# Kernel optimization log

Hardware: AMD Instinct MI355X
Metric: run time of the kernel (lower is better)

The kernel has to match this reference:

```python
import jax, jax.numpy as jnp
import numpy as np
import math

B, T, C = 4, 2048, 1024
N_HEADS = 16
D_HEAD = C // N_HEADS


def _rope_tables(d_head, max_seq_len):
    half = d_head // 2
    theta = 1.0 / (10000.0 ** (jnp.arange(half, dtype=jnp.float32) / half))
    pos = jnp.arange(max_seq_len, dtype=jnp.float32)
    freqs = jnp.outer(pos, theta)  # [S, half]
    cos = jnp.concatenate([jnp.cos(freqs), jnp.cos(freqs)], axis=-1)  # [S, d_head]
    sin = jnp.concatenate([jnp.sin(freqs), jnp.sin(freqs)], axis=-1)
    return cos, sin


def _rotate_half(x):
    d = x.shape[-1] // 2
    return jnp.concatenate([-x[..., d:], x[..., :d]], axis=-1)


def _apply_rope(x, cos, sin):
    # x: [B, H, T, d_head]; cos/sin: [T, d_head] broadcast over B,H
    return x * cos[None, None] + _rotate_half(x) * sin[None, None]


def setup_inputs() -> dict:
    key = jax.random.key(0)
    k1, k2, k3 = jax.random.split(key, 3)
    x = jax.random.normal(k1, (B, T, C), dtype=jnp.float32)
    W_qkv = jax.random.normal(k2, (C, 3 * C), dtype=jnp.float32) * (1.0 / math.sqrt(C))
    W_proj = jax.random.normal(k3, (C, C), dtype=jnp.float32) * (1.0 / math.sqrt(C))
    return {"x": x, "W_qkv": W_qkv, "W_proj": W_proj}


def reference(x, W_qkv, W_proj):
    b, t, c = x.shape
    qkv = x @ W_qkv  # [B, T, 3C]
    q, k, v = jnp.split(qkv, 3, axis=-1)

    def reshape(z):
        return z.reshape(b, t, N_HEADS, D_HEAD).transpose(0, 2, 1, 3)  # [B,H,T,dh]

    q, k, v = reshape(q), reshape(k), reshape(v)

    cos, sin = _rope_tables(D_HEAD, t)
    q = _apply_rope(q, cos, sin)
    k = _apply_rope(k, cos, sin)

    scale = 1.0 / math.sqrt(D_HEAD)
    att = jnp.einsum('bhqd,bhkd->bhqk', q, k) * scale  # [B,H,T,T]
    causal = jnp.tril(jnp.ones((t, t), dtype=bool))
    att = jnp.where(causal[None, None], att, -jnp.inf)
    att = jax.nn.softmax(att, axis=-1)
    out = jnp.einsum('bhqk,bhkd->bhqd', att, v)  # [B,H,T,dh]
    out = out.transpose(0, 2, 1, 3).reshape(b, t, c)
    return out @ W_proj
```

## Files before the change

kernel.cpp:

```cpp
#include <hip/hip_runtime.h>
#include <stdint.h>

#define Bz 4
#define Tz 2048
#define Cz 1024
#define NHz 16
#define DHz 64
#define Mz (Bz*Tz)

typedef unsigned short u16;
typedef __attribute__((ext_vector_type(8))) short short8;
typedef __attribute__((ext_vector_type(8))) unsigned short ushort8v;
typedef __attribute__((ext_vector_type(4))) unsigned short u16x4;
typedef __attribute__((ext_vector_type(4))) float f32x4;
typedef __attribute__((ext_vector_type(2))) unsigned int uint2v;

__device__ __forceinline__ float bf2f(u16 u){
  union { unsigned int i; float f; } v; v.i = ((unsigned int)u) << 16; return v.f;
}
__device__ __forceinline__ u16 f2bf(float f){
  union { float f; unsigned int i; } v; v.f = f;
  unsigned int r = v.i + 0x7FFFu + ((v.i >> 16) & 1u);
  return (u16)(r >> 16);
}


__global__ void k_cast_bf16(const float* __restrict__ in, u16* __restrict__ out, int n4){
  int i = blockIdx.x*256 + threadIdx.x;
  if (i >= n4) return;
  float4 v = ((const float4*)in)[i];
  u16x4 o;
  o[0] = f2bf(v.x); o[1] = f2bf(v.y); o[2] = f2bf(v.z); o[3] = f2bf(v.w);
  *(u16x4*)(out + (size_t)i*4) = o;
}

__global__ void k_transpose_cast(const float* __restrict__ W, u16* __restrict__ Wt, int K, int N){
  __shared__ float tile[32][33];
  int n0 = blockIdx.x*32, k0 = blockIdx.y*32;
  int tx = threadIdx.x, ty = threadIdx.y;
  #pragma unroll
  for (int i = 0; i < 32; i += 8)
    tile[ty+i][tx] = W[(size_t)(k0+ty+i)*N + n0 + tx];
  __syncthreads();
  #pragma unroll
  for (int i = 0; i < 32; i += 8)
    Wt[(size_t)(n0+ty+i)*K + k0 + tx] = f2bf(tile[tx][ty+i]);
}

__global__ void k_rope_tables(float* __restrict__ cosT, float* __restrict__ sinT){
  int idx = blockIdx.x*256 + threadIdx.x;
  int t = idx >> 5, i = idx & 31;
  float theta = exp2f(-(float)i * (13.287712379549449f / 32.0f));
  float ang = (float)t * theta;
  cosT[idx] = cosf(ang);
  sinT[idx] = sinf(ang);
}

#define GLDS(src, dstE) __builtin_amdgcn_global_load_lds( \
    (const __attribute__((address_space(1))) unsigned int*)(src), \
    (__attribute__((address_space(3))) unsigned int*)((u16*)lds + (dstE)), 16, 0, 0)

template<int Nn, int Kk, bool ROPE>
__global__ __launch_bounds__(256, 4) void k_gemmdb(const u16* __restrict__ A, const u16* __restrict__ Bt,
                        void* __restrict__ Cout, u16* __restrict__ vTout,
                        const float* __restrict__ cosT, const float* __restrict__ sinT){
  __shared__ u16 lds[2][16384];
  constexpr int NT = Kk/64;
  const int bm = blockIdx.x, bn = blockIdx.y;
  const int tid = threadIdx.x, lane = tid & 63, w = tid >> 6;
  const int wm = (w >> 1)*64, wn = (w & 1)*64;
  const int g = lane >> 4, r = lane & 15;

  const int srow8 = lane >> 3;
  const int sslot = (lane & 7) ^ srow8;
  const u16* asrc = A  + (size_t)(bm*128 + w*32 + srow8)*Kk + sslot*8;
  const u16* bsrc = Bt + (size_t)(bn*128 + w*32 + srow8)*Kk + sslot*8;
  const int dA = w*2048 + lane*8;
  const int dB = 8192 + w*2048 + lane*8;

  int a_off[4][2], b_off[4][2];
  #pragma unroll
  for (int i = 0; i < 4; ++i)
    #pragma unroll
    for (int kc = 0; kc < 2; ++kc){
      int row = wm + i*16 + r;
      a_off[i][kc] = (row*128 + kc*64 + g*16) ^ ((r & 7) << 4);
      int rowb = wn + i*16 + r;
      b_off[i][kc] = 16384 + ((rowb*128 + kc*64 + g*16) ^ ((r & 7) << 4));
    }

  f32x4 acc[4][4] = {};

#define STG(t, bi) do{ \
    const size_t ko_ = (size_t)(t)*64; \
    const int be_ = (bi)*16384; \
    GLDS(asrc + ko_,                 be_ + dA);        \
    GLDS(asrc + ko_ +  8*(size_t)Kk, be_ + dA + 512);  \
    GLDS(asrc + ko_ + 16*(size_t)Kk, be_ + dA + 1024); \
    GLDS(asrc + ko_ + 24*(size_t)Kk, be_ + dA + 1536); \
    GLDS(bsrc + ko_,                 be_ + dB);        \
    GLDS(bsrc + ko_ +  8*(size_t)Kk, be_ + dB + 512);  \
    GLDS(bsrc + ko_ + 16*(size_t)Kk, be_ + dB + 1024); \
    GLDS(bsrc + ko_ + 24*(size_t)Kk, be_ + dB + 1536); \
  }while(0)

  STG(0, 0);
  asm volatile("s_waitcnt vmcnt(0)" ::: "memory");
  __builtin_amdgcn_s_barrier();

  int buf = 0;
  #pragma unroll 1
  for (int t = 0; t < NT; ++t){
    if (t + 1 < NT) STG(t+1, buf^1);
    const char* Lb = (const char*)lds + buf*32768;
    short8 af[4][2], bf[4][2];
    #pragma unroll
    for (int i = 0; i < 4; ++i)
      #pragma unroll
      for (int kc = 0; kc < 2; ++kc){
        af[i][kc] = *(const short8*)(Lb + a_off[i][kc]);
        bf[i][kc] = *(const short8*)(Lb + b_off[i][kc]);
      }
    __builtin_amdgcn_s_setprio(1);
    #pragma unroll
    for (int i = 0; i < 4; ++i)
      #pragma unroll
      for (int j = 0; j < 4; ++j){
        acc[i][j] = __builtin_amdgcn_mfma_f32_16x16x32_bf16(af[i][0], bf[j][0], acc[i][j], 0,0,0);
        acc[i][j] = __builtin_amdgcn_mfma_f32_16x16x32_bf16(af[i][1], bf[j][1], acc[i][j], 0,0,0);
      }
    __builtin_amdgcn_s_setprio(0);
    if (t + 1 < NT){
      asm volatile("s_waitcnt vmcnt(0)" ::: "memory");
      __builtin_amdgcn_s_barrier();
      buf ^= 1;
    }
  }
#undef STG

  const int nbase = bn*128 + wn;
  if (ROPE && nbase >= 2048){
    const int b = bm >> 4;
    const int h = (nbase >> 6) & 15;
    #pragma unroll
    for (int ri = 0; ri < 4; ++ri){
      const int m0 = bm*128 + wm + ri*16 + 4*g;
      const int t0 = m0 & (Tz-1);
      #pragma unroll
      for (int cj = 0; cj < 4; ++cj){
        const int d = cj*16 + r;
        u16x4 o;
        #pragma unroll
        for (int jj = 0; jj < 4; ++jj) o[jj] = f2bf(acc[ri][cj][jj]);
        *(u16x4*)(vTout + ((size_t)((b*16 + h)*64 + d))*2048 + t0) = o;
      }
    }
  } else if (ROPE){
    const float qs = (nbase < 1024) ? 0.18033688011112042f : 1.0f;
    #pragma unroll
    for (int ri = 0; ri < 4; ++ri)
      #pragma unroll
      for (int jj = 0; jj < 4; ++jj){
        const int m = bm*128 + wm + ri*16 + 4*g + jj;
        const int t = m & (Tz-1);
        #pragma unroll
        for (int cj = 0; cj < 2; ++cj){
          const int ch = cj*16 + r;
          float cv = cosT[t*32 + ch];
          float sv = sinT[t*32 + ch];
          float lo = acc[ri][cj][jj], hi = acc[ri][cj+2][jj];
          ((u16*)Cout)[(size_t)m*Nn + nbase + ch]      = f2bf((lo*cv - hi*sv)*qs);
          ((u16*)Cout)[(size_t)m*Nn + nbase + ch + 32] = f2bf((hi*cv + lo*sv)*qs);
        }
      }
  } else {
    #pragma unroll
    for (int ri = 0; ri < 4; ++ri)
      #pragma unroll
      for (int cj = 0; cj < 4; ++cj)
        #pragma unroll
        for (int jj = 0; jj < 4; ++jj){
          const size_t m = bm*128 + wm + ri*16 + 4*g + jj;
          const size_t n = (size_t)nbase + cj*16 + r;
          ((float*)Cout)[m*Nn + n] = acc[ri][cj][jj];
        }
  }
}

__global__ __launch_bounds__(512) void k_attn2(const u16* __restrict__ qkv,
                                               const u16* __restrict__ vT,
                                               u16* __restrict__ att){
  __shared__ u16 K_lds[2*4096];
  __shared__ u16 V_lds[2*4096];
  __shared__ u16 P_lds[8*16*72];

  const int bh = blockIdx.x;
  const int b = bh >> 4, h = bh & 15;
  const int tid = threadIdx.x;
  const int w = tid >> 6;
  const int lane = tid & 63;
  const int g = lane >> 4;
  const int ql = lane & 15;
  u16* Pw = P_lds + w*16*72;

  const int srow  = lane >> 3;
  const int sslot = (lane & 7) ^ srow;
  const u16* ksrc = qkv + ((size_t)(b*Tz + 8*w + srow))*3072 + 1024 + h*64 + sslot*8;
  const u16* vsrc = vT  + ((size_t)bh*64 + 8*w + srow)*2048 + sslot*8;
  u16* kdst = K_lds + w*512 + lane*8;
  u16* vdst = V_lds + w*512 + lane*8;

  short8 ones;
  #pragma unroll
  for (int i = 0; i < 8; ++i) ones[i] = (short)0x3F80;

  int fofs[4][2];
  #pragma unroll
  for (int t = 0; t < 4; ++t){
    int row = 16*t + ql;
    fofs[t][0] = (row*128 + 16*g)      ^ ((row & 7) << 4);
    fofs[t][1] = (row*128 + 64 + 16*g) ^ ((row & 7) << 4);
  }

  #pragma unroll 1
  for (int half = 0; half < 2; ++half){
    const int qt = (half == 0) ? blockIdx.y : (15 - blockIdx.y);
    const int qr0w = qt*128 + w*16;
    const int nt = 2*qt + 2;

    const u16* qsrc = qkv + (size_t)(b*Tz + qr0w + ql)*3072 + h*64;
    short8 qf0 = *(const short8*)(qsrc + g*8);
    short8 qf1 = *(const short8*)(qsrc + 32 + g*8);

    f32x4 acc[4] = {{0,0,0,0},{0,0,0,0},{0,0,0,0},{0,0,0,0}};
    f32x4 accl = {0,0,0,0};

    __builtin_amdgcn_global_load_lds(
      (const __attribute__((address_space(1))) unsigned int*)(ksrc),
      (__attribute__((address_space(3))) unsigned int*)(kdst), 16, 0, 0);
    __builtin_amdgcn_global_load_lds(
      (const __attribute__((address_space(1))) unsigned int*)(vsrc),
      (__attribute__((address_space(3))) unsigned int*)(vdst), 16, 0, 0);
    __syncthreads();

    #pragma unroll 2
    for (int kt = 0; kt < nt; ++kt){
      const int buf = kt & 1;
      if (kt + 1 < nt){
        __builtin_amdgcn_global_load_lds(
          (const __attribute__((address_space(1))) unsigned int*)(ksrc + (size_t)(kt+1)*64*3072),
          (__attribute__((address_space(3))) unsigned int*)(kdst + (buf^1)*4096), 16, 0, 0);
        __builtin_amdgcn_global_load_lds(
          (const __attribute__((address_space(1))) unsigned int*)(vsrc + (kt+1)*64),
          (__attribute__((address_space(3))) unsigned int*)(vdst + (buf^1)*4096), 16, 0, 0);
      }
      const char* Kb = (const char*)(K_lds + buf*4096);
      const char* Vb = (const char*)(V_lds + buf*4096);
      const int kv0 = kt*64;

      f32x4 st[4];
      __builtin_amdgcn_s_setprio(1);
      #pragma unroll
      for (int t = 0; t < 4; ++t){
        short8 kf0 = *(const short8*)(Kb + fofs[t][0]);
        short8 kf1 = *(const short8*)(Kb + fofs[t][1]);
        f32x4 z = {0,0,0,0};
        z = __builtin_amdgcn_mfma_f32_16x16x32_bf16(kf0, qf0, z, 0, 0, 0);
        z = __builtin_amdgcn_mfma_f32_16x16x32_bf16(kf1, qf1, z, 0, 0, 0);
        st[t] = z;
      }
      __builtin_amdgcn_s_setprio(0);

      if (kv0 + 63 > qr0w){
        const int qg = qr0w + ql;
        #pragma unroll
        for (int t = 0; t < 4; ++t)
          #pragma unroll
          for (int j = 0; j < 4; ++j)
            if (kv0 + 16*t + 4*g + j > qg) st[t][j] = -1e30f;
      }

      #pragma unroll
      for (int t = 0; t < 4; ++t){
        float p0, p1, p2, p3;
        asm("v_exp_f32 %0, %1" : "=v"(p0) : "v"(st[t][0]));
        asm("v_exp_f32 %0, %1" : "=v"(p1) : "v"(st[t][1]));
        asm("v_exp_f32 %0, %1" : "=v"(p2) : "v"(st[t][2]));
        asm("v_exp_f32 %0, %1" : "=v"(p3) : "v"(st[t][3]));
        unsigned int lov, hiv;
        asm("v_cvt_pk_bf16_f32 %0, %1, %2" : "=v"(lov) : "v"(p0), "v"(p1));
        asm("v_cvt_pk_bf16_f32 %0, %1, %2" : "=v"(hiv) : "v"(p2), "v"(p3));
        uint2v pv; pv[0] = lov; pv[1] = hiv;
        *(uint2v*)((char*)Pw + ql*144 + (16*t + 4*g)*2) = pv;
      }

      short8 pf0 = *(const short8*)((char*)Pw + ql*144 + 16*g);
      short8 pf1 = *(const short8*)((char*)Pw + ql*144 + 64 + 16*g);
      __builtin_amdgcn_s_setprio(1);
      accl = __builtin_amdgcn_mfma_f32_16x16x32_bf16(pf0, ones, accl, 0, 0, 0);
      accl = __builtin_amdgcn_mfma_f32_16x16x32_bf16(pf1, ones, accl, 0, 0, 0);
      #pragma unroll
      for (int dt = 0; dt < 4; ++dt){
        short8 vf0 = *(const short8*)(Vb + fofs[dt][0]);
        short8 vf1 = *(const short8*)(Vb + fofs[dt][1]);
        acc[dt] = __builtin_amdgcn_mfma_f32_16x16x32_bf16(pf0, vf0, acc[dt], 0, 0, 0);
        acc[dt] = __builtin_amdgcn_mfma_f32_16x16x32_bf16(pf1, vf1, acc[dt], 0, 0, 0);
      }
      __builtin_amdgcn_s_setprio(0);
      __syncthreads();
    }

    float lj[4];
    #pragma unroll
    for (int j = 0; j < 4; ++j) lj[j] = 1.0f / accl[j];
    #pragma unroll
    for (int dt = 0; dt < 4; ++dt)
      #pragma unroll
      for (int j = 0; j < 4; ++j)
        att[(size_t)(b*Tz + qr0w + 4*g + j)*Cz + h*64 + dt*16 + ql] = f2bf(acc[dt][j]*lj[j]);
  }
}


extern "C" void kernel_launch(void* const* d_in, const int* in_sizes, int n_in,
                              void* d_out, int out_size, void* d_ws, size_t ws_size,
                              hipStream_t stream){
  const float* x     = (const float*)d_in[0];
  const float* Wqkv  = (const float*)d_in[1];
  const float* Wproj = (const float*)d_in[2];
  float* out = (float*)d_out;
  char* ws = (char*)d_ws;

  u16*  xb   = (u16*)(ws);
  u16*  wqt  = (u16*)(ws + 16777216);
  u16*  wpt  = (u16*)(ws + 23068672);
  u16*  qkv  = (u16*)(ws + 25165824);
  u16*  vTr  = (u16*)(ws + 75497472);
  float* cosT = (float*)(ws + 92274688);
  float* sinT = (float*)(ws + 92536832);

  k_cast_bf16<<<Mz*Cz/4/256, 256, 0, stream>>>(x, xb, Mz*Cz/4);
  k_transpose_cast<<<dim3(3072/32, 1024/32), dim3(32,8), 0, stream>>>(Wqkv, wqt, 1024, 3072);
  k_transpose_cast<<<dim3(1024/32, 1024/32), dim3(32,8), 0, stream>>>(Wproj, wpt, 1024, 1024);
  k_rope_tables<<<Tz*32/256, 256, 0, stream>>>(cosT, sinT);

  k_gemmdb<3072, 1024, true><<<dim3(Mz/128, 3072/128), 256, 0, stream>>>(
      xb, wqt, qkv, vTr, cosT, sinT);
  k_attn2<<<dim3(Bz*NHz, 8), 512, 0, stream>>>(qkv, vTr, xb);
  k_gemmdb<1024, 1024, false><<<dim3(Mz/128, 1024/128), 256, 0, stream>>>(
      xb, wpt, out, nullptr, nullptr, nullptr);
}
```

Before: 157.9 us.

## Process two 16-row query tiles per wave and compute softmax row sums with VALU

The attention kernel now runs 256 threads (4 waves), and each wave handles 32 query rows as two 16-row MFMA tiles that share every K and V fragment read from LDS. The ones-vector MFMA that produced softmax row sums is replaced by per-lane VALU adds followed by cross-lane shuffles at the end. The aim is to halve LDS fragment traffic per unit of MFMA work and to drop the extra MFMAs. In exchange the kernel uses more registers and has fewer waves per block, which could reduce latency hiding.

```diff
diff --git a/kernel.cpp b/kernel.cpp
--- a/kernel.cpp
+++ b/kernel.cpp
@@ -187,12 +187,12 @@
   }
 }
 
-__global__ __launch_bounds__(512) void k_attn2(const u16* __restrict__ qkv,
+__global__ __launch_bounds__(256) void k_attn3(const u16* __restrict__ qkv,
                                                const u16* __restrict__ vT,
                                                u16* __restrict__ att){
   __shared__ u16 K_lds[2*4096];
   __shared__ u16 V_lds[2*4096];
-  __shared__ u16 P_lds[8*16*72];
+  __shared__ u16 P_lds[4*32*72];
 
   const int bh = blockIdx.x;
   const int b = bh >> 4, h = bh & 15;
@@ -201,18 +201,14 @@
   const int lane = tid & 63;
   const int g = lane >> 4;
   const int ql = lane & 15;
-  u16* Pw = P_lds + w*16*72;
+  u16* Pw = P_lds + w*32*72;
 
   const int srow  = lane >> 3;
   const int sslot = (lane & 7) ^ srow;
-  const u16* ksrc = qkv + ((size_t)(b*Tz + 8*w + srow))*3072 + 1024 + h*64 + sslot*8;
-  const u16* vsrc = vT  + ((size_t)bh*64 + 8*w + srow)*2048 + sslot*8;
-  u16* kdst = K_lds + w*512 + lane*8;
-  u16* vdst = V_lds + w*512 + lane*8;
-
-  short8 ones;
-  #pragma unroll
-  for (int i = 0; i < 8; ++i) ones[i] = (short)0x3F80;
+  const u16* ksrc = qkv + ((size_t)(b*Tz + 16*w + srow))*3072 + 1024 + h*64 + sslot*8;
+  const u16* vsrc = vT  + ((size_t)bh*64 + 16*w + srow)*2048 + sslot*8;
+  u16* kdst = K_lds + w*1024 + lane*8;
+  u16* vdst = V_lds + w*1024 + lane*8;
 
   int fofs[4][2];
   #pragma unroll
@@ -222,52 +218,63 @@
     fofs[t][1] = (row*128 + 64 + 16*g) ^ ((row & 7) << 4);
   }
 
+#define STG_KV(kt, bi) do{ \
+    const u16* ks_ = ksrc + (size_t)(kt)*64*3072; \
+    const u16* vs_ = vsrc + (kt)*64; \
+    u16* kd_ = kdst + (bi)*4096; \
+    u16* vd_ = vdst + (bi)*4096; \
+    __builtin_amdgcn_global_load_lds((const __attribute__((address_space(1))) unsigned int*)(ks_), \
+        (__attribute__((address_space(3))) unsigned int*)(kd_), 16, 0, 0); \
+    __builtin_amdgcn_global_load_lds((const __attribute__((address_space(1))) unsigned int*)(ks_ + 8*3072), \
+        (__attribute__((address_space(3))) unsigned int*)(kd_ + 512), 16, 0, 0); \
+    __builtin_amdgcn_global_load_lds((const __attribute__((address_space(1))) unsigned int*)(vs_), \
+        (__attribute__((address_space(3))) unsigned int*)(vd_), 16, 0, 0); \
+    __builtin_amdgcn_global_load_lds((const __attribute__((address_space(1))) unsigned int*)(vs_ + 8*2048), \
+        (__attribute__((address_space(3))) unsigned int*)(vd_ + 512), 16, 0, 0); \
+  }while(0)
+
   #pragma unroll 1
   for (int half = 0; half < 2; ++half){
     const int qt = (half == 0) ? blockIdx.y : (15 - blockIdx.y);
-    const int qr0w = qt*128 + w*16;
+    const int qr0w = qt*128 + w*32;
     const int nt = 2*qt + 2;
 
-    const u16* qsrc = qkv + (size_t)(b*Tz + qr0w + ql)*3072 + h*64;
-    short8 qf0 = *(const short8*)(qsrc + g*8);
-    short8 qf1 = *(const short8*)(qsrc + 32 + g*8);
-
-    f32x4 acc[4] = {{0,0,0,0},{0,0,0,0},{0,0,0,0},{0,0,0,0}};
-    f32x4 accl = {0,0,0,0};
-
-    __builtin_amdgcn_global_load_lds(
-      (const __attribute__((address_space(1))) unsigned int*)(ksrc),
-      (__attribute__((address_space(3))) unsigned int*)(kdst), 16, 0, 0);
-    __builtin_amdgcn_global_load_lds(
-      (const __attribute__((address_space(1))) unsigned int*)(vsrc),
-      (__attribute__((address_space(3))) unsigned int*)(vdst), 16, 0, 0);
+    const u16* qsrcA = qkv + (size_t)(b*Tz + qr0w + ql)*3072 + h*64;
+    const u16* qsrcB = qsrcA + 16*3072;
+    short8 qfA0 = *(const short8*)(qsrcA + g*8);
+    short8 qfA1 = *(const short8*)(qsrcA + 32 + g*8);
+    short8 qfB0 = *(const short8*)(qsrcB + g*8);
+    short8 qfB1 = *(const short8*)(qsrcB + 32 + g*8);
+
+    f32x4 accA[4] = {{0,0,0,0},{0,0,0,0},{0,0,0,0},{0,0,0,0}};
+    f32x4 accB[4] = {{0,0,0,0},{0,0,0,0},{0,0,0,0},{0,0,0,0}};
+    float lrA = 0.0f, lrB = 0.0f;
+
+    STG_KV(0, 0);
     __syncthreads();
 
     #pragma unroll 2
     for (int kt = 0; kt < nt; ++kt){
       const int buf = kt & 1;
-      if (kt + 1 < nt){
-        __builtin_amdgcn_global_load_lds(
-          (const __attribute__((address_space(1))) unsigned int*)(ksrc + (size_t)(kt+1)*64*3072),
-          (__attribute__((address_space(3))) unsigned int*)(kdst + (buf^1)*4096), 16, 0, 0);
-        __builtin_amdgcn_global_load_lds(
-          (const __attribute__((address_space(1))) unsigned int*)(vsrc + (kt+1)*64),
-          (__attribute__((address_space(3))) unsigned int*)(vdst + (buf^1)*4096), 16, 0, 0);
-      }
+      if (kt + 1 < nt) STG_KV(kt+1, buf^1);
       const char* Kb = (const char*)(K_lds + buf*4096);
       const char* Vb = (const char*)(V_lds + buf*4096);
       const int kv0 = kt*64;
 
-      f32x4 st[4];
+      f32x4 stA[4], stB[4];
       __builtin_amdgcn_s_setprio(1);
       #pragma unroll
       for (int t = 0; t < 4; ++t){
         short8 kf0 = *(const short8*)(Kb + fofs[t][0]);
         short8 kf1 = *(const short8*)(Kb + fofs[t][1]);
-        f32x4 z = {0,0,0,0};
-        z = __builtin_amdgcn_mfma_f32_16x16x32_bf16(kf0, qf0, z, 0, 0, 0);
-        z = __builtin_amdgcn_mfma_f32_16x16x32_bf16(kf1, qf1, z, 0, 0, 0);
-        st[t] = z;
+        f32x4 zA = {0,0,0,0};
+        zA = __builtin_amdgcn_mfma_f32_16x16x32_bf16(kf0, qfA0, zA, 0, 0, 0);
+        zA = __builtin_amdgcn_mfma_f32_16x16x32_bf16(kf1, qfA1, zA, 0, 0, 0);
+        stA[t] = zA;
+        f32x4 zB = {0,0,0,0};
+        zB = __builtin_amdgcn_mfma_f32_16x16x32_bf16(kf0, qfB0, zB, 0, 0, 0);
+        zB = __builtin_amdgcn_mfma_f32_16x16x32_bf16(kf1, qfB1, zB, 0, 0, 0);
+        stB[t] = zB;
       }
       __builtin_amdgcn_s_setprio(0);
 
@@ -277,48 +284,80 @@
         for (int t = 0; t < 4; ++t)
           #pragma unroll
           for (int j = 0; j < 4; ++j)
-            if (kv0 + 16*t + 4*g + j > qg) st[t][j] = -1e30f;
+            if (kv0 + 16*t + 4*g + j > qg) stA[t][j] = -1e30f;
+      }
+      if (kv0 + 63 > qr0w + 16){
+        const int qg = qr0w + 16 + ql;
+        #pragma unroll
+        for (int t = 0; t < 4; ++t)
+          #pragma unroll
+          for (int j = 0; j < 4; ++j)
+            if (kv0 + 16*t + 4*g + j > qg) stB[t][j] = -1e30f;
       }
 
       #pragma unroll
       for (int t = 0; t < 4; ++t){
-        float p0, p1, p2, p3;
-        asm("v_exp_f32 %0, %1" : "=v"(p0) : "v"(st[t][0]));
-        asm("v_exp_f32 %0, %1" : "=v"(p1) : "v"(st[t][1]));
-        asm("v_exp_f32 %0, %1" : "=v"(p2) : "v"(st[t][2]));
-        asm("v_exp_f32 %0, %1" : "=v"(p3) : "v"(st[t][3]));
-        unsigned int lov, hiv;
-        asm("v_cvt_pk_bf16_f32 %0, %1, %2" : "=v"(lov) : "v"(p0), "v"(p1));
-        asm("v_cvt_pk_bf16_f32 %0, %1, %2" : "=v"(hiv) : "v"(p2), "v"(p3));
-        uint2v pv; pv[0] = lov; pv[1] = hiv;
-        *(uint2v*)((char*)Pw + ql*144 + (16*t + 4*g)*2) = pv;
-      }
-
-      short8 pf0 = *(const short8*)((char*)Pw + ql*144 + 16*g);
-      short8 pf1 = *(const short8*)((char*)Pw + ql*144 + 64 + 16*g);
+        float a0, a1, a2, a3, b0, b1, b2, b3;
+        asm("v_exp_f32 %0, %1" : "=v"(a0) : "v"(stA[t][0]));
+        asm("v_exp_f32 %0, %1" : "=v"(a1) : "v"(stA[t][1]));
+        asm("v_exp_f32 %0, %1" : "=v"(a2) : "v"(stA[t][2]));
+        asm("v_exp_f32 %0, %1" : "=v"(a3) : "v"(stA[t][3]));
+        asm("v_exp_f32 %0, %1" : "=v"(b0) : "v"(stB[t][0]));
+        asm("v_exp_f32 %0, %1" : "=v"(b1) : "v"(stB[t][1]));
+        asm("v_exp_f32 %0, %1" : "=v"(b2) : "v"(stB[t][2]));
+        asm("v_exp_f32 %0, %1" : "=v"(b3) : "v"(stB[t][3]));
+        lrA += (a0+a1)+(a2+a3);
+        lrB += (b0+b1)+(b2+b3);
+        unsigned int wa0, wa1, wb0, wb1;
+        asm("v_cvt_pk_bf16_f32 %0, %1, %2" : "=v"(wa0) : "v"(a0), "v"(a1));
+        asm("v_cvt_pk_bf16_f32 %0, %1, %2" : "=v"(wa1) : "v"(a2), "v"(a3));
+        asm("v_cvt_pk_bf16_f32 %0, %1, %2" : "=v"(wb0) : "v"(b0), "v"(b1));
+        asm("v_cvt_pk_bf16_f32 %0, %1, %2" : "=v"(wb1) : "v"(b2), "v"(b3));
+        uint2v pva; pva[0] = wa0; pva[1] = wa1;
+        uint2v pvb; pvb[0] = wb0; pvb[1] = wb1;
+        *(uint2v*)((char*)Pw + ql*144 + (16*t + 4*g)*2) = pva;
+        *(uint2v*)((char*)Pw + (16 + ql)*144 + (16*t + 4*g)*2) = pvb;
+      }
+
+      short8 pfA0 = *(const short8*)((char*)Pw + ql*144 + 16*g);
+      short8 pfA1 = *(const short8*)((char*)Pw + ql*144 + 64 + 16*g);
+      short8 pfB0 = *(const short8*)((char*)Pw + (16 + ql)*144 + 16*g);
+      short8 pfB1 = *(const short8*)((char*)Pw + (16 + ql)*144 + 64 + 16*g);
+
       __builtin_amdgcn_s_setprio(1);
-      accl = __builtin_amdgcn_mfma_f32_16x16x32_bf16(pf0, ones, accl, 0, 0, 0);
-      accl = __builtin_amdgcn_mfma_f32_16x16x32_bf16(pf1, ones, accl, 0, 0, 0);
       #pragma unroll
       for (int dt = 0; dt < 4; ++dt){
         short8 vf0 = *(const short8*)(Vb + fofs[dt][0]);
         short8 vf1 = *(const short8*)(Vb + fofs[dt][1]);
-        acc[dt] = __builtin_amdgcn_mfma_f32_16x16x32_bf16(pf0, vf0, acc[dt], 0, 0, 0);
-        acc[dt] = __builtin_amdgcn_mfma_f32_16x16x32_bf16(pf1, vf1, acc[dt], 0, 0, 0);
+        accA[dt] = __builtin_amdgcn_mfma_f32_16x16x32_bf16(pfA0, vf0, accA[dt], 0, 0, 0);
+        accA[dt] = __builtin_amdgcn_mfma_f32_16x16x32_bf16(pfA1, vf1, accA[dt], 0, 0, 0);
+        accB[dt] = __builtin_amdgcn_mfma_f32_16x16x32_bf16(pfB0, vf0, accB[dt], 0, 0, 0);
+        accB[dt] = __builtin_amdgcn_mfma_f32_16x16x32_bf16(pfB1, vf1, accB[dt], 0, 0, 0);
       }
       __builtin_amdgcn_s_setprio(0);
       __syncthreads();
     }
 
-    float lj[4];
-    #pragma unroll
-    for (int j = 0; j < 4; ++j) lj[j] = 1.0f / accl[j];
-    #pragma unroll
-    for (int dt = 0; dt < 4; ++dt)
-      #pragma unroll
-      for (int j = 0; j < 4; ++j)
-        att[(size_t)(b*Tz + qr0w + 4*g + j)*Cz + h*64 + dt*16 + ql] = f2bf(acc[dt][j]*lj[j]);
+    lrA += __shfl_xor(lrA, 16); lrA += __shfl_xor(lrA, 32);
+    lrB += __shfl_xor(lrB, 16); lrB += __shfl_xor(lrB, 32);
+    float liA = 1.0f / lrA;
+    float liB = 1.0f / lrB;
+    float lA0 = __shfl(liA, 4*g+0), lA1 = __shfl(liA, 4*g+1);
+    float lA2 = __shfl(liA, 4*g+2), lA3 = __shfl(liA, 4*g+3);
+    float lB0 = __shfl(liB, 4*g+0), lB1 = __shfl(liB, 4*g+1);
+    float lB2 = __shfl(liB, 4*g+2), lB3 = __shfl(liB, 4*g+3);
+    #pragma unroll
+    for (int dt = 0; dt < 4; ++dt){
+      float ljA[4] = {lA0, lA1, lA2, lA3};
+      float ljB[4] = {lB0, lB1, lB2, lB3};
+      #pragma unroll
+      for (int j = 0; j < 4; ++j){
+        att[(size_t)(b*Tz + qr0w + 4*g + j)*Cz + h*64 + dt*16 + ql]      = f2bf(accA[dt][j]*ljA[j]);
+        att[(size_t)(b*Tz + qr0w + 16 + 4*g + j)*Cz + h*64 + dt*16 + ql] = f2bf(accB[dt][j]*ljB[j]);
+      }
+    }
   }
+#undef STG_KV
 }
 
 
@@ -346,7 +385,7 @@
 
   k_gemmdb<3072, 1024, true><<<dim3(Mz/128, 3072/128), 256, 0, stream>>>(
       xb, wqt, qkv, vTr, cosT, sinT);
-  k_attn2<<<dim3(Bz*NHz, 8), 512, 0, stream>>>(qkv, vTr, xb);
+  k_attn3<<<dim3(Bz*NHz, 8), 256, 0, stream>>>(qkv, vTr, xb);
   k_gemmdb<1024, 1024, false><<<dim3(Mz/128, 1024/128), 256, 0, stream>>>(
       xb, wpt, out, nullptr, nullptr, nullptr);
 }
```

Result: slower. 172.7 us (+9.3%).
